# Optimization experiments

Measured on AMD Instinct MI355X. Metric: run time of the kernel, lower is better.

The kernel has to match this reference:

```python
import jax, jax.numpy as jnp
import numpy as np
import math

B, S, D, H = 32, 512, 1024, 1024


def setup_inputs() -> dict:
    key = jax.random.key(0)
    k_feats, k_wih, k_whh, k_bih, k_bhh = jax.random.split(key, 5)
    stdv = 1.0 / math.sqrt(H)
    u = lambda k, shape: jax.random.uniform(k, shape, jnp.float32, -stdv, stdv)
    return {
        "feats": jax.random.normal(k_feats, (B, S, D), jnp.float32),
        "weight_ih": u(k_wih, (3 * H, D)),
        "weight_hh": u(k_whh, (3 * H, H)),
        "bias_ih": u(k_bih, (3 * H,)),
        "bias_hh": u(k_bhh, (3 * H,)),
    }


def reference(feats, weight_ih, weight_hh, bias_ih, bias_hh):
    b, s, d = feats.shape
    h_dim = weight_hh.shape[1]
    # Precompute input projections for all timesteps in one GEMM: [B,S,3H]
    gi_all = jnp.einsum('bsd,gd->bsg', feats, weight_ih) + bias_ih

    def step(h, gi_t):
        gh = h @ weight_hh.T + bias_hh  # [B,3H]
        i_r, i_i, i_n = jnp.split(gi_t, 3, axis=-1)
        h_r, h_i, h_n = jnp.split(gh, 3, axis=-1)
        resetgate = jax.nn.sigmoid(i_r + h_r)
        inputgate = jax.nn.sigmoid(i_i + h_i)
        newgate = jnp.tanh(i_n + resetgate * h_n)
        hy = newgate + inputgate * (h - newgate)
        return hy, hy

    h0 = jnp.zeros((b, h_dim), feats.dtype)
    h_last, outs = jax.lax.scan(step, h0, jnp.swapaxes(gi_all, 0, 1))  # outs: [S,B,H]
    output = jnp.swapaxes(outs, 0, 1)  # [B,S,H]
    return output, h_last
```

## Files before the change

kernel.cpp:

```cpp
#include <hip/hip_runtime.h>

#define B_  32
#define S_  512
#define D_  1024
#define H_  1024
#define G3  3072

typedef __attribute__((ext_vector_type(8))) short  short8;
typedef __attribute__((ext_vector_type(4))) float  floatx4;

__device__ __forceinline__ unsigned short f2bf(float f) {
    unsigned int u = __builtin_bit_cast(unsigned int, f);
    u = (u + 0x7FFFu + ((u >> 16) & 1u)) >> 16;
    return (unsigned short)u;
}
__device__ __forceinline__ float bf2f(unsigned short h) {
    unsigned int u = ((unsigned int)h) << 16;
    return __builtin_bit_cast(float, u);
}
__device__ __forceinline__ float fsigmoid(float x) {
    float e = __builtin_amdgcn_exp2f(-1.4426950408889634f * x);
    return __builtin_amdgcn_rcpf(1.f + e);
}
__device__ __forceinline__ float ftanh(float x) {
    float e = __builtin_amdgcn_exp2f(2.8853900817779268f * x);
    return 1.f - 2.f * __builtin_amdgcn_rcpf(e + 1.f);
}

__global__ __launch_bounds__(256) void convert_kernel(
    const float* __restrict__ wih, const float* __restrict__ whh,
    unsigned short* __restrict__ wih_h,
    unsigned short* __restrict__ whh_h, unsigned short* __restrict__ whh_l,
    unsigned int* __restrict__ hbuf ,
    int* __restrict__ cnt ) {
    int tid = blockIdx.x * 256 + threadIdx.x;
    int i4 = tid * 4;
    if (i4 < 3145728) {
        float4 w = *(const float4*)(wih + i4);
        ushort4 o;
        o.x = f2bf(w.x); o.y = f2bf(w.y); o.z = f2bf(w.z); o.w = f2bf(w.w);
        *(ushort4*)(wih_h + i4) = o;

        float4 v = *(const float4*)(whh + i4);
        ushort4 h;
        h.x = f2bf(v.x); h.y = f2bf(v.y); h.z = f2bf(v.z); h.w = f2bf(v.w);
        ushort4 l;
        l.x = f2bf(v.x - bf2f(h.x)); l.y = f2bf(v.y - bf2f(h.y));
        l.z = f2bf(v.z - bf2f(h.z)); l.w = f2bf(v.w - bf2f(h.w));
        *(ushort4*)(whh_h + i4) = h;
        *(ushort4*)(whh_l + i4) = l;
    }
    if (tid < 16384) {
        uint4 z; z.x = z.y = z.z = z.w = 0;
        *(uint4*)(hbuf + tid * 4) = z;
    }
    if (tid < 32) {
        int4 z4; z4.x = z4.y = z4.z = z4.w = 0;
        *(int4*)(cnt + tid * 4) = z4;
    }
}

#define BM 128
#define BN 128
#define BK 32
#define LDA 40

__global__ __launch_bounds__(256, 2) void gi_gemm(
    const float* __restrict__ feats,
    const unsigned short* __restrict__ wih_h,
    const float* __restrict__ bias_ih,
    unsigned short* __restrict__ gi) {
    __shared__ unsigned short As[BM * LDA];
    __shared__ unsigned short Bs[BN * LDA];

    int bx = blockIdx.x;
    int nb = bx % (G3 / BN);
    int mb = bx / (G3 / BN);
    int m0 = mb * BM, n0 = nb * BN;
    int tid = threadIdx.x;
    int lane = tid & 63, wave = tid >> 6;
    int quad = lane >> 4, l15 = lane & 15;
    int wm = (wave >> 1) * 64, wn = (wave & 1) * 64;

    floatx4 acc[4][4];
#pragma unroll
    for (int i = 0; i < 4; ++i)
#pragma unroll
        for (int j = 0; j < 4; ++j) acc[i][j] = (floatx4){0.f, 0.f, 0.f, 0.f};

    float bias[4];
#pragma unroll
    for (int j = 0; j < 4; ++j) bias[j] = bias_ih[n0 + wn + j * 16 + l15];

    int srow = tid >> 1, shalf = tid & 1;
    const float* aptr = feats + (size_t)(m0 + srow) * D_ + shalf * 16;
    const unsigned short* bptr = wih_h + (size_t)(n0 + srow) * D_ + shalf * 16;
    unsigned short* as = As + srow * LDA + shalf * 16;
    unsigned short* bs = Bs + srow * LDA + shalf * 16;

    for (int kt = 0; kt < D_ / BK; ++kt) {
        int k0 = kt * BK;
        float4 a0 = *(const float4*)(aptr + k0);
        float4 a1 = *(const float4*)(aptr + k0 + 4);
        float4 a2 = *(const float4*)(aptr + k0 + 8);
        float4 a3 = *(const float4*)(aptr + k0 + 12);
        uint4 bA = *(const uint4*)(bptr + k0);
        uint4 bB = *(const uint4*)(bptr + k0 + 8);

        union { unsigned short u16[16]; uint4 v[2]; } pk;
        pk.u16[0] = f2bf(a0.x);  pk.u16[1] = f2bf(a0.y);
        pk.u16[2] = f2bf(a0.z);  pk.u16[3] = f2bf(a0.w);
        pk.u16[4] = f2bf(a1.x);  pk.u16[5] = f2bf(a1.y);
        pk.u16[6] = f2bf(a1.z);  pk.u16[7] = f2bf(a1.w);
        pk.u16[8] = f2bf(a2.x);  pk.u16[9] = f2bf(a2.y);
        pk.u16[10] = f2bf(a2.z); pk.u16[11] = f2bf(a2.w);
        pk.u16[12] = f2bf(a3.x); pk.u16[13] = f2bf(a3.y);
        pk.u16[14] = f2bf(a3.z); pk.u16[15] = f2bf(a3.w);

        *(uint4*)as = pk.v[0];
        *(uint4*)(as + 8) = pk.v[1];
        *(uint4*)bs = bA;
        *(uint4*)(bs + 8) = bB;
        __syncthreads();

        short8 af[4], bf[4];
#pragma unroll
        for (int i = 0; i < 4; ++i)
            af[i] = *(const short8*)(As + (wm + i * 16 + l15) * LDA + quad * 8);
#pragma unroll
        for (int j = 0; j < 4; ++j)
            bf[j] = *(const short8*)(Bs + (wn + j * 16 + l15) * LDA + quad * 8);
#pragma unroll
        for (int i = 0; i < 4; ++i)
#pragma unroll
            for (int j = 0; j < 4; ++j)
                acc[i][j] = __builtin_amdgcn_mfma_f32_16x16x32_bf16(
                    af[i], bf[j], acc[i][j], 0, 0, 0);
        __syncthreads();
    }

#pragma unroll
    for (int i = 0; i < 4; ++i)
#pragma unroll
        for (int j = 0; j < 4; ++j)
#pragma unroll
            for (int r = 0; r < 4; ++r) {
                int m = m0 + wm + i * 16 + quad * 4 + r;
                int n = n0 + wn + j * 16 + l15;
                gi[(size_t)m * G3 + n] = f2bf(acc[i][j][r] + bias[j]);
            }
}

__global__ __launch_bounds__(512, 2) void gru_rec(
    const unsigned short* __restrict__ gi,
    const unsigned short* __restrict__ whh_h,
    const unsigned short* __restrict__ whh_l,
    const float* __restrict__ bias_hh,
    unsigned int* __restrict__ hbuf,
    int* __restrict__ cnt,
    float* __restrict__ out) {
    __shared__ floatx4 parts[8][3][64];

    int jg = blockIdx.x >> 1, mt = blockIdx.x & 1;
    int tid = threadIdx.x;
    int ks = tid >> 6, lane = tid & 63;
    int quad = lane >> 4, l15 = lane & 15;
    int j = jg * 16 + l15;

    short8 wfh[3][4], wfl[3][4];
#pragma unroll
    for (int g = 0; g < 3; ++g)
#pragma unroll
        for (int ki = 0; ki < 4; ++ki) {
            size_t off = (size_t)(g * H_ + j) * H_ + ks * 128 + ki * 32 + quad * 8;
            wfh[g][ki] = *(const short8*)(whh_h + off);
            wfl[g][ki] = *(const short8*)(whh_l + off);
        }

    float bhh[3] = {0.f, 0.f, 0.f};
    float hreg[4] = {0.f, 0.f, 0.f, 0.f};
    if (ks == 0) {
#pragma unroll
        for (int g = 0; g < 3; ++g) bhh[g] = bias_hh[g * H_ + j];
    }

    const int arow = mt * 16 + l15;
    const int kbase = ks * 128 + quad * 8;
    int* const cbase = cnt + mt * 64;

    for (int t = 0; t < S_; ++t) {
        unsigned short giu[3][4];
        if (ks == 0) {
#pragma unroll
            for (int g = 0; g < 3; ++g)
#pragma unroll
                for (int r = 0; r < 4; ++r) {
                    int b = mt * 16 + quad * 4 + r;
                    giu[g][r] = gi[((size_t)b * S_ + t) * G3 + g * H_ + j];
                }
        }

        if (t > 0) {
            if (ks == 0) {
                int v = __hip_atomic_load(cbase + lane, __ATOMIC_RELAXED,
                                          __HIP_MEMORY_SCOPE_AGENT);
                while (!__all(v >= t)) {
                    __builtin_amdgcn_s_sleep(1);
                    v = __hip_atomic_load(cbase + lane, __ATOMIC_RELAXED,
                                          __HIP_MEMORY_SCOPE_AGENT);
                }
            }
            __syncthreads();
        }

        const unsigned int* hc = hbuf + ((t & 1) << 15);
        unsigned int* hn = hbuf + (((t & 1) ^ 1) << 15);

        short8 ah[4], al[4];
#pragma unroll
        for (int ki = 0; ki < 4; ++ki) {
            const unsigned long long* p =
                (const unsigned long long*)(hc + arow * H_ + kbase + ki * 32);
            unsigned long long q[4];
#pragma unroll
            for (int c = 0; c < 4; ++c)
                q[c] = __hip_atomic_load(p + c, __ATOMIC_RELAXED,
                                         __HIP_MEMORY_SCOPE_AGENT);
            short8 av, lv;
#pragma unroll
            for (int c = 0; c < 4; ++c) {
                unsigned int u0 = (unsigned int)q[c];
                unsigned int u1 = (unsigned int)(q[c] >> 32);
                av[2 * c]     = (short)(u0 & 0xffffu);
                av[2 * c + 1] = (short)(u1 & 0xffffu);
                lv[2 * c]     = (short)(u0 >> 16);
                lv[2 * c + 1] = (short)(u1 >> 16);
            }
            ah[ki] = av;
            al[ki] = lv;
        }

        floatx4 acc[3];
#pragma unroll
        for (int g = 0; g < 3; ++g) acc[g] = (floatx4){0.f, 0.f, 0.f, 0.f};
#pragma unroll
        for (int ki = 0; ki < 4; ++ki)
#pragma unroll
            for (int g = 0; g < 3; ++g) {
                acc[g] = __builtin_amdgcn_mfma_f32_16x16x32_bf16(ah[ki], wfh[g][ki], acc[g], 0, 0, 0);
                acc[g] = __builtin_amdgcn_mfma_f32_16x16x32_bf16(ah[ki], wfl[g][ki], acc[g], 0, 0, 0);
                acc[g] = __builtin_amdgcn_mfma_f32_16x16x32_bf16(al[ki], wfh[g][ki], acc[g], 0, 0, 0);
            }
#pragma unroll
        for (int g = 0; g < 3; ++g) parts[ks][g][lane] = acc[g];
        __syncthreads();

        float hy[4];
        if (ks == 0) {
            floatx4 gh[3];
#pragma unroll
            for (int g = 0; g < 3; ++g) {
                floatx4 s = parts[0][g][lane];
#pragma unroll
                for (int w = 1; w < 8; ++w) s += parts[w][g][lane];
                gh[g] = s;
            }
#pragma unroll
            for (int r = 0; r < 4; ++r) {
                int b = mt * 16 + quad * 4 + r;
                float rg = fsigmoid(bf2f(giu[0][r]) + gh[0][r] + bhh[0]);
                float zg = fsigmoid(bf2f(giu[1][r]) + gh[1][r] + bhh[1]);
                float ng = ftanh(bf2f(giu[2][r]) + rg * (gh[2][r] + bhh[2]));
                float h = ng + zg * (hreg[r] - ng);
                hreg[r] = h;
                hy[r] = h;
                unsigned short hh = f2bf(h);
                unsigned int pk = (unsigned int)hh |
                                  ((unsigned int)f2bf(h - bf2f(hh)) << 16);
                __hip_atomic_store(hn + b * H_ + j, pk, __ATOMIC_RELAXED,
                                   __HIP_MEMORY_SCOPE_AGENT);
            }
            asm volatile("s_waitcnt vmcnt(0)" ::: "memory");
            if (tid == 0)
                __hip_atomic_store(cbase + jg, t + 1, __ATOMIC_RELAXED,
                                   __HIP_MEMORY_SCOPE_AGENT);
#pragma unroll
            for (int r = 0; r < 4; ++r) {
                int b = mt * 16 + quad * 4 + r;
                __builtin_nontemporal_store(hy[r], out + ((size_t)b * S_ + t) * H_ + j);
                if (t == S_ - 1)
                    __builtin_nontemporal_store(hy[r], out + (size_t)B_ * S_ * H_ + (size_t)b * H_ + j);
            }
        }
    }
}

extern "C" void kernel_launch(void* const* d_in, const int* in_sizes, int n_in,
                              void* d_out, int out_size, void* d_ws, size_t ws_size,
                              hipStream_t stream) {
    const float* feats = (const float*)d_in[0];
    const float* wih   = (const float*)d_in[1];
    const float* whh   = (const float*)d_in[2];
    const float* bih   = (const float*)d_in[3];
    const float* bhh   = (const float*)d_in[4];
    float* out = (float*)d_out;

    unsigned short* wih_h = (unsigned short*)d_ws;
    unsigned short* whh_h = wih_h + (size_t)3145728;
    unsigned short* whh_l = whh_h + (size_t)3145728;
    unsigned short* gi    = whh_l + (size_t)3145728;
    unsigned int*   hbuf  = (unsigned int*)(gi + (size_t)16384 * G3);
    int*            cnt   = (int*)(hbuf + 65536);

    hipLaunchKernelGGL(convert_kernel, dim3(3072), dim3(256), 0, stream,
                       wih, whh, wih_h, whh_h, whh_l, hbuf, cnt);
    hipLaunchKernelGGL(gi_gemm, dim3(3072), dim3(256), 0, stream,
                       feats, wih_h, bih, gi);

    void* args[] = {(void*)&gi, (void*)&whh_h, (void*)&whh_l,
                    (void*)&bhh, (void*)&hbuf, (void*)&cnt, (void*)&out};
    hipLaunchCooperativeKernel((const void*)gru_rec, dim3(128), dim3(512),
                               args, 0, stream);
}
```

Baseline: 3.451 ms.

## Pipeline GRU recurrence over four batch slices with padded per-slice flags

The recurrent kernel drops to 64 blocks, each owning 16 hidden columns for all 32 batch rows. The batch is split into four 8-row slices processed in a rotating four-phase pipeline. While one slice's MFMA and gate finalisation run, other waves prefetch the next slice's hidden state and input projections and poll the readiness flags for the slice two phases ahead, hiding cross-block synchronisation latency. The flags are padded to one per 128 bytes to avoid false sharing. In exchange, half the MFMA rows are wasted on zero-padded 8-row tiles, and each block does four times as many barriers per step.

```diff
diff --git a/kernel.cpp b/kernel.cpp
--- a/kernel.cpp
+++ b/kernel.cpp
@@ -54,7 +54,7 @@
         uint4 z; z.x = z.y = z.z = z.w = 0;
         *(uint4*)(hbuf + tid * 4) = z;
     }
-    if (tid < 32) {
+    if (tid < 2048) {
         int4 z4; z4.x = z4.y = z4.z = z4.w = 0;
         *(int4*)(cnt + tid * 4) = z4;
     }
@@ -160,12 +160,13 @@
     int* __restrict__ cnt,
     float* __restrict__ out) {
     __shared__ floatx4 parts[8][3][64];
-
-    int jg = blockIdx.x >> 1, mt = blockIdx.x & 1;
-    int tid = threadIdx.x;
-    int ks = tid >> 6, lane = tid & 63;
-    int quad = lane >> 4, l15 = lane & 15;
-    int j = jg * 16 + l15;
+    const float* const pf = (const float*)parts;
+
+    const int tid = threadIdx.x;
+    const int lane = tid & 63, ks = tid >> 6;
+    const int quad = lane >> 4, l15 = lane & 15;
+    const int jg = blockIdx.x;
+    const int j = jg * 16 + l15;
 
     short8 wfh[3][4], wfl[3][4];
 #pragma unroll
@@ -177,122 +178,151 @@
             wfl[g][ki] = *(const short8*)(whh_l + off);
         }
 
-    float bhh[3] = {0.f, 0.f, 0.f};
-    float hreg[4] = {0.f, 0.f, 0.f, 0.f};
-    if (ks == 0) {
-#pragma unroll
-        for (int g = 0; g < 3; ++g) bhh[g] = bias_hh[g * H_ + j];
-    }
-
-    const int arow = mt * 16 + l15;
+    const int rr = tid >> 4, cc = tid & 15;
+    const int jc = jg * 16 + cc;
+    float bR = 0.f, bZ = 0.f, bN = 0.f;
+    float hr0 = 0.f, hr1 = 0.f, hr2 = 0.f, hr3 = 0.f;
+    if (tid < 128) {
+        bR = bias_hh[jc]; bZ = bias_hh[H_ + jc]; bN = bias_hh[2 * H_ + jc];
+    }
+
     const int kbase = ks * 128 + quad * 8;
-    int* const cbase = cnt + mt * 64;
+    const int lidx = ((rr >> 2) * 16 + cc);
+    const int r4 = rr & 3;
+
+    short8 ahA[4], alA[4], ahB[4], alB[4];
+    const short8 z8 = (short8){0, 0, 0, 0, 0, 0, 0, 0};
+#pragma unroll
+    for (int ki = 0; ki < 4; ++ki) { ahA[ki] = z8; alA[ki] = z8;
+                                     ahB[ki] = z8; alB[ki] = z8; }
+    unsigned short gAr = 0, gAz = 0, gAn = 0, gBr = 0, gBz = 0, gBn = 0;
+
+#define LOADH(SN, TL, AH, AL)                                                  \
+    if (l15 < 8) {                                                             \
+        const unsigned long long* p = (const unsigned long long*)(hbuf +       \
+            ((size_t)((TL) & 1) << 15) + (size_t)((SN) * 8 + l15) * H_ + kbase); \
+        unsigned long long q[16];                                              \
+        _Pragma("unroll")                                                      \
+        for (int ki = 0; ki < 4; ++ki)                                         \
+            _Pragma("unroll")                                                  \
+            for (int c = 0; c < 4; ++c)                                        \
+                q[ki * 4 + c] = __hip_atomic_load(p + ki * 16 + c,             \
+                    __ATOMIC_RELAXED, __HIP_MEMORY_SCOPE_AGENT);               \
+        _Pragma("unroll")                                                      \
+        for (int ki = 0; ki < 4; ++ki) {                                       \
+            short8 av, lv;                                                     \
+            _Pragma("unroll")                                                  \
+            for (int c = 0; c < 4; ++c) {                                      \
+                unsigned long long qq = q[ki * 4 + c];                         \
+                unsigned int u0 = (unsigned int)qq;                            \
+                unsigned int u1 = (unsigned int)(qq >> 32);                    \
+                av[2 * c]     = (short)(u0 & 0xffffu);                         \
+                av[2 * c + 1] = (short)(u1 & 0xffffu);                         \
+                lv[2 * c]     = (short)(u0 >> 16);                             \
+                lv[2 * c + 1] = (short)(u1 >> 16);                             \
+            }                                                                  \
+            AH[ki] = av; AL[ki] = lv;                                          \
+        }                                                                      \
+    }
+
+#define LOADGI(SN, TL, GR, GZ, GN)                                             \
+    {                                                                          \
+        const size_t gb = ((size_t)((SN) * 8 + rr) * S_ + (TL)) * G3 + jc;     \
+        GR = gi[gb]; GZ = gi[gb + H_]; GN = gi[gb + 2 * H_];                   \
+    }
+
+#define MFMAB(AH, AL)                                                          \
+    {                                                                          \
+        floatx4 acc[3];                                                        \
+        _Pragma("unroll")                                                      \
+        for (int g = 0; g < 3; ++g) acc[g] = (floatx4){0.f, 0.f, 0.f, 0.f};    \
+        _Pragma("unroll")                                                      \
+        for (int ki = 0; ki < 4; ++ki)                                         \
+            _Pragma("unroll")                                                  \
+            for (int g = 0; g < 3; ++g) {                                      \
+                acc[g] = __builtin_amdgcn_mfma_f32_16x16x32_bf16(AH[ki], wfh[g][ki], acc[g], 0, 0, 0); \
+                acc[g] = __builtin_amdgcn_mfma_f32_16x16x32_bf16(AH[ki], wfl[g][ki], acc[g], 0, 0, 0); \
+                acc[g] = __builtin_amdgcn_mfma_f32_16x16x32_bf16(AL[ki], wfh[g][ki], acc[g], 0, 0, 0); \
+            }                                                                  \
+        _Pragma("unroll")                                                      \
+        for (int g = 0; g < 3; ++g) parts[ks][g][lane] = acc[g];               \
+    }
+
+#define FIN(P, GR, GZ, GN, HR)                                                 \
+    {                                                                          \
+        float gh0 = 0.f, gh1 = 0.f, gh2 = 0.f;                                 \
+        _Pragma("unroll")                                                      \
+        for (int w = 0; w < 8; ++w) {                                          \
+            gh0 += pf[(((w * 3 + 0) * 64 + lidx) << 2) + r4];                  \
+            gh1 += pf[(((w * 3 + 1) * 64 + lidx) << 2) + r4];                  \
+            gh2 += pf[(((w * 3 + 2) * 64 + lidx) << 2) + r4];                  \
+        }                                                                      \
+        const float rg = fsigmoid(bf2f(GR) + gh0 + bR);                        \
+        const float zg = fsigmoid(bf2f(GZ) + gh1 + bZ);                        \
+        const float ng = ftanh(bf2f(GN) + rg * (gh2 + bN));                    \
+        const float hy = ng + zg * (HR - ng);                                  \
+        HR = hy;                                                               \
+        const unsigned short hh = f2bf(hy);                                    \
+        const unsigned int pk = (unsigned int)hh |                             \
+                                ((unsigned int)f2bf(hy - bf2f(hh)) << 16);     \
+        const int brow = (P) * 8 + rr;                                         \
+        __hip_atomic_store(hbuf + ((size_t)((t + 1) & 1) << 15) +              \
+                           (size_t)brow * H_ + jc, pk,                         \
+                           __ATOMIC_RELAXED, __HIP_MEMORY_SCOPE_AGENT);        \
+        asm volatile("s_waitcnt vmcnt(0)" ::: "memory");                       \
+        if (tid == 0)                                                          \
+            __hip_atomic_store(cnt + ((P) * 64 + jg) * 32, t + 1,              \
+                               __ATOMIC_RELAXED, __HIP_MEMORY_SCOPE_AGENT);    \
+        __builtin_nontemporal_store(hy, out + ((size_t)brow * S_ + t) * H_ + jc); \
+        if (t == S_ - 1)                                                       \
+            __builtin_nontemporal_store(hy,                                    \
+                out + (size_t)B_ * S_ * H_ + (size_t)brow * H_ + jc);          \
+    }
+
+#define POLLF(SS, TP)                                                          \
+    {                                                                          \
+        const int* fp = cnt + ((SS) * 64 + lane) * 32;                         \
+        int v = __hip_atomic_load(fp, __ATOMIC_RELAXED,                        \
+                                  __HIP_MEMORY_SCOPE_AGENT);                   \
+        while (!__all(v >= (TP))) {                                            \
+            __builtin_amdgcn_s_sleep(1);                                       \
+            v = __hip_atomic_load(fp, __ATOMIC_RELAXED,                        \
+                                  __HIP_MEMORY_SCOPE_AGENT);                   \
+        }                                                                      \
+    }
+
+#define PHASE(P, AHC, ALC, AHN, ALN, GCr, GCz, GCn, GNr, GNz, GNn, HR)         \
+    {                                                                          \
+        const int TL = t + ((P) == 3 ? 1 : 0);                                 \
+        if (ks >= 2 && TL < S_) { LOADH((((P) + 1) & 3), TL, AHN, ALN); }      \
+        MFMAB(AHC, ALC);                                                       \
+        __syncthreads();                                                       \
+        if (ks < 2) {                                                          \
+            FIN(P, GCr, GCz, GCn, HR);                                         \
+            if (TL < S_) {                                                     \
+                LOADH((((P) + 1) & 3), TL, AHN, ALN);                          \
+                LOADGI((((P) + 1) & 3), TL, GNr, GNz, GNn);                    \
+            }                                                                  \
+        } else if (ks == 2) {                                                  \
+            POLLF((((P) + 2) & 3), t + ((P) >= 2 ? 1 : 0));                    \
+        }                                                                      \
+        __syncthreads();                                                       \
+    }
+
+    if (tid < 128) { LOADGI(0, 0, gAr, gAz, gAn); }
 
     for (int t = 0; t < S_; ++t) {
-        unsigned short giu[3][4];
-        if (ks == 0) {
-#pragma unroll
-            for (int g = 0; g < 3; ++g)
-#pragma unroll
-                for (int r = 0; r < 4; ++r) {
-                    int b = mt * 16 + quad * 4 + r;
-                    giu[g][r] = gi[((size_t)b * S_ + t) * G3 + g * H_ + j];
-                }
-        }
-
-        if (t > 0) {
-            if (ks == 0) {
-                int v = __hip_atomic_load(cbase + lane, __ATOMIC_RELAXED,
-                                          __HIP_MEMORY_SCOPE_AGENT);
-                while (!__all(v >= t)) {
-                    __builtin_amdgcn_s_sleep(1);
-                    v = __hip_atomic_load(cbase + lane, __ATOMIC_RELAXED,
-                                          __HIP_MEMORY_SCOPE_AGENT);
-                }
-            }
-            __syncthreads();
-        }
-
-        const unsigned int* hc = hbuf + ((t & 1) << 15);
-        unsigned int* hn = hbuf + (((t & 1) ^ 1) << 15);
-
-        short8 ah[4], al[4];
-#pragma unroll
-        for (int ki = 0; ki < 4; ++ki) {
-            const unsigned long long* p =
-                (const unsigned long long*)(hc + arow * H_ + kbase + ki * 32);
-            unsigned long long q[4];
-#pragma unroll
-            for (int c = 0; c < 4; ++c)
-                q[c] = __hip_atomic_load(p + c, __ATOMIC_RELAXED,
-                                         __HIP_MEMORY_SCOPE_AGENT);
-            short8 av, lv;
-#pragma unroll
-            for (int c = 0; c < 4; ++c) {
-                unsigned int u0 = (unsigned int)q[c];
-                unsigned int u1 = (unsigned int)(q[c] >> 32);
-                av[2 * c]     = (short)(u0 & 0xffffu);
-                av[2 * c + 1] = (short)(u1 & 0xffffu);
-                lv[2 * c]     = (short)(u0 >> 16);
-                lv[2 * c + 1] = (short)(u1 >> 16);
-            }
-            ah[ki] = av;
-            al[ki] = lv;
-        }
-
-        floatx4 acc[3];
-#pragma unroll
-        for (int g = 0; g < 3; ++g) acc[g] = (floatx4){0.f, 0.f, 0.f, 0.f};
-#pragma unroll
-        for (int ki = 0; ki < 4; ++ki)
-#pragma unroll
-            for (int g = 0; g < 3; ++g) {
-                acc[g] = __builtin_amdgcn_mfma_f32_16x16x32_bf16(ah[ki], wfh[g][ki], acc[g], 0, 0, 0);
-                acc[g] = __builtin_amdgcn_mfma_f32_16x16x32_bf16(ah[ki], wfl[g][ki], acc[g], 0, 0, 0);
-                acc[g] = __builtin_amdgcn_mfma_f32_16x16x32_bf16(al[ki], wfh[g][ki], acc[g], 0, 0, 0);
-            }
-#pragma unroll
-        for (int g = 0; g < 3; ++g) parts[ks][g][lane] = acc[g];
-        __syncthreads();
-
-        float hy[4];
-        if (ks == 0) {
-            floatx4 gh[3];
-#pragma unroll
-            for (int g = 0; g < 3; ++g) {
-                floatx4 s = parts[0][g][lane];
-#pragma unroll
-                for (int w = 1; w < 8; ++w) s += parts[w][g][lane];
-                gh[g] = s;
-            }
-#pragma unroll
-            for (int r = 0; r < 4; ++r) {
-                int b = mt * 16 + quad * 4 + r;
-                float rg = fsigmoid(bf2f(giu[0][r]) + gh[0][r] + bhh[0]);
-                float zg = fsigmoid(bf2f(giu[1][r]) + gh[1][r] + bhh[1]);
-                float ng = ftanh(bf2f(giu[2][r]) + rg * (gh[2][r] + bhh[2]));
-                float h = ng + zg * (hreg[r] - ng);
-                hreg[r] = h;
-                hy[r] = h;
-                unsigned short hh = f2bf(h);
-                unsigned int pk = (unsigned int)hh |
-                                  ((unsigned int)f2bf(h - bf2f(hh)) << 16);
-                __hip_atomic_store(hn + b * H_ + j, pk, __ATOMIC_RELAXED,
-                                   __HIP_MEMORY_SCOPE_AGENT);
-            }
-            asm volatile("s_waitcnt vmcnt(0)" ::: "memory");
-            if (tid == 0)
-                __hip_atomic_store(cbase + jg, t + 1, __ATOMIC_RELAXED,
-                                   __HIP_MEMORY_SCOPE_AGENT);
-#pragma unroll
-            for (int r = 0; r < 4; ++r) {
-                int b = mt * 16 + quad * 4 + r;
-                __builtin_nontemporal_store(hy[r], out + ((size_t)b * S_ + t) * H_ + j);
-                if (t == S_ - 1)
-                    __builtin_nontemporal_store(hy[r], out + (size_t)B_ * S_ * H_ + (size_t)b * H_ + j);
-            }
-        }
-    }
+        PHASE(0, ahA, alA, ahB, alB, gAr, gAz, gAn, gBr, gBz, gBn, hr0);
+        PHASE(1, ahB, alB, ahA, alA, gBr, gBz, gBn, gAr, gAz, gAn, hr1);
+        PHASE(2, ahA, alA, ahB, alB, gAr, gAz, gAn, gBr, gBz, gBn, hr2);
+        PHASE(3, ahB, alB, ahA, alA, gBr, gBz, gBn, gAr, gAz, gAn, hr3);
+    }
+#undef LOADH
+#undef LOADGI
+#undef MFMAB
+#undef FIN
+#undef POLLF
+#undef PHASE
 }
 
 extern "C" void kernel_launch(void* const* d_in, const int* in_sizes, int n_in,
@@ -319,6 +349,6 @@
 
     void* args[] = {(void*)&gi, (void*)&whh_h, (void*)&whh_l,
                     (void*)&bhh, (void*)&hbuf, (void*)&cnt, (void*)&out};
-    hipLaunchCooperativeKernel((const void*)gru_rec, dim3(128), dim3(512),
+    hipLaunchCooperativeKernel((const void*)gru_rec, dim3(64), dim3(512),
                                args, 0, stream);
 }
```

Result: slower. 8.550 ms (+147.8%).
